# Optimization experiments

Hardware: AMD Instinct MI355X
Metric: run time of the kernel (lower is better)

Reference implementation:

```python
import jax, jax.numpy as jnp
import numpy as np

K = 20  # kNN fan-out


def knn_idx(x, k):
    # x: (B, C, N). Negative squared pairwise distance; top-k largest = nearest.
    inner = -2.0 * jnp.einsum('bcn,bcm->bnm', x, x)        # (B, N, N)
    xx = jnp.sum(x * x, axis=1)                            # (B, N)
    pd = -xx[:, :, None] - inner - xx[:, None, :]          # (B, N, N)
    return jax.lax.top_k(pd, k)[1]                         # (B, N, k) int32


def get_graph_feature(x, k):
    # x: (B, C, N) -> edge features (B, 2C, N, k)
    idx = knn_idx(x, k)                                    # (B, N, k)
    xt = jnp.transpose(x, (0, 2, 1))                       # (B, N, C)
    nbrs = jax.vmap(lambda pts, ids: pts[ids])(xt, idx)    # (B, N, k, C)
    center = xt[:, :, None, :]                             # (B, N, 1, C)
    feat = jnp.concatenate(
        [nbrs - center, jnp.broadcast_to(center, nbrs.shape)], axis=-1)  # (B,N,k,2C)
    return jnp.transpose(feat, (0, 3, 1, 2))               # (B, 2C, N, k)


def vn_layer(W, x):
    # W: (out, in); x: (B, in, N, k) -> (B, out, N, k)
    return jnp.einsum('oi,bink->bonk', W, x)


def setup_inputs() -> dict:
    key = jax.random.key(0)
    ks = jax.random.split(key, 6)
    B, C, N = 16, 3, 2048
    num_classes = 10
    return {
        'x': jax.random.normal(ks[0], (B, C, N), dtype=jnp.float32),
        'W1': jax.random.normal(ks[1], (64, 6), dtype=jnp.float32),
        'W2': jax.random.normal(ks[2], (128, 64), dtype=jnp.float32),
        'W3': jax.random.normal(ks[3], (256, 128), dtype=jnp.float32),
        'fc_w': jax.random.normal(ks[4], (num_classes, 256), dtype=jnp.float32) * 0.0625,
        'fc_b': jax.random.normal(ks[5], (num_classes,), dtype=jnp.float32) * 0.0625,
    }


def reference(x, W1, W2, W3, fc_w, fc_b):
    h = get_graph_feature(x, K)          # (B, 6, N, k)
    h = vn_layer(W1, h)                  # (B, 64, N, k)
    h = jax.nn.relu(vn_layer(W2, h))     # (B, 128, N, k)
    h = jax.nn.relu(vn_layer(W3, h))     # (B, 256, N, k)
    h = jnp.max(h, axis=-1)              # max over neighbors k -> (B, 256, N)
    h = jnp.max(h, axis=-1)              # global max over points -> (B, 256)
    return h @ fc_w.T + fc_b             # (B, num_classes)
```

## Files before the change

kernel.cpp:

```cpp
#include <hip/hip_runtime.h>
#include <stdint.h>

typedef _Float16 v8h __attribute__((ext_vector_type(8)));
typedef _Float16 v2h __attribute__((ext_vector_type(2)));
typedef float v4f __attribute__((ext_vector_type(4)));
typedef float v16f __attribute__((ext_vector_type(16)));

#define NPTS 2048
#define BATCH 16
#define KNN 20
#define PAIRS (NPTS * KNN)

__device__ __forceinline__ unsigned pair_relu_h2(unsigned pu, unsigned qu) {
  v2h a = *(const v2h*)&pu;
  v2h b = *(const v2h*)&qu;
  v2h s = a + b;
  v2h z = {(_Float16)0.f, (_Float16)0.f};
  v2h r = __builtin_elementwise_max(s, z);
  return *(const unsigned*)&r;
}

__global__ void prep_kernel(const float* __restrict__ W1, const float* __restrict__ W2,
                            float* __restrict__ M2a, float* __restrict__ M2b,
                            int* __restrict__ H) {
  if (blockIdx.x == 0 && threadIdx.x < 128) {
    int o = threadIdx.x;
    float a0 = 0, a1 = 0, a2 = 0, b0 = 0, b1 = 0, b2 = 0;
    for (int i = 0; i < 64; ++i) {
      float w2 = W2[o * 64 + i];
      const float* w1r = W1 + i * 6;
      a0 += w2 * w1r[0]; a1 += w2 * w1r[1]; a2 += w2 * w1r[2];
      b0 += w2 * (w1r[3] - w1r[0]); b1 += w2 * (w1r[4] - w1r[1]); b2 += w2 * (w1r[5] - w1r[2]);
    }
    M2a[o * 3 + 0] = a0; M2a[o * 3 + 1] = a1; M2a[o * 3 + 2] = a2;
    M2b[o * 3 + 0] = b0; M2b[o * 3 + 1] = b1; M2b[o * 3 + 2] = b2;
  }
  int g = blockIdx.x * 128 + threadIdx.x;
  if (g < BATCH * 256) H[g] = 0;
}

__global__ __launch_bounds__(64) void pq_kernel(const float* __restrict__ x,
                                                const float* __restrict__ M2a,
                                                const float* __restrict__ M2b,
                                                unsigned short* __restrict__ p,
                                                unsigned short* __restrict__ q) {
  int b = blockIdx.x >> 6;
  int j0 = (blockIdx.x & 63) << 5;
  int t = threadIdx.x;
  int o0 = t * 2;
  float a00 = M2a[o0 * 3 + 0], a01 = M2a[o0 * 3 + 1], a02 = M2a[o0 * 3 + 2];
  float a10 = M2a[o0 * 3 + 3], a11 = M2a[o0 * 3 + 4], a12 = M2a[o0 * 3 + 5];
  float b00 = M2b[o0 * 3 + 0], b01 = M2b[o0 * 3 + 1], b02 = M2b[o0 * 3 + 2];
  float b10 = M2b[o0 * 3 + 3], b11 = M2b[o0 * 3 + 4], b12 = M2b[o0 * 3 + 5];
  const float* xb = x + b * 3 * NPTS;
  unsigned* pw = (unsigned*)p;
  unsigned* qw = (unsigned*)q;
  for (int jj = 0; jj < 32; ++jj) {
    int j = j0 + jj;
    float x0 = xb[j], x1 = xb[NPTS + j], x2 = xb[2 * NPTS + j];
    float p0 = a00 * x0 + a01 * x1 + a02 * x2;
    float p1 = a10 * x0 + a11 * x1 + a12 * x2;
    float q0 = b00 * x0 + b01 * x1 + b02 * x2;
    float q1 = b10 * x0 + b11 * x1 + b12 * x2;
    size_t base = ((size_t)(b * NPTS + j)) * 64 + t;
    auto hp = __builtin_amdgcn_cvt_pkrtz(p0, p1);
    auto hq = __builtin_amdgcn_cvt_pkrtz(q0, q1);
    pw[base] = *(const unsigned*)&hp;
    qw[base] = *(const unsigned*)&hq;
  }
}

__global__ __launch_bounds__(256) void knn_kernel(const float* __restrict__ x,
                                                  int* __restrict__ idxOut) {
  __shared__ float px[NPTS], py[NPTS], pz[NPTS];
  __shared__ unsigned long long cand[4][4][128];
  int b = blockIdx.x >> 7;
  int qblk = blockIdx.x & 127;
  const float* xb = x + b * 3 * NPTS;
  for (int i = threadIdx.x; i < NPTS; i += 256) {
    px[i] = xb[i]; py[i] = xb[NPTS + i]; pz[i] = xb[2 * NPTS + i];
  }
  __syncthreads();
  int wid = threadIdx.x >> 6, lane = threadIdx.x & 63;
  int qbase = qblk * 16 + wid * 4;

  float qx[4], qy[4], qz[4], mn[4];
#pragma unroll
  for (int g = 0; g < 4; ++g) {
    qx[g] = px[qbase + g]; qy[g] = py[qbase + g]; qz[g] = pz[qbase + g];
    mn[g] = 1e30f;
  }

  for (int s = 0; s < 32; ++s) {
    int i = s * 64 + lane;
    float X = px[i], Y = py[i], Z = pz[i];
#pragma unroll
    for (int g = 0; g < 4; ++g) {
      float dx = X - qx[g], dy = Y - qy[g], dz = Z - qz[g];
      mn[g] = fminf(mn[g], dx * dx + dy * dy + dz * dz);
    }
  }

  float tau[4];
#pragma unroll
  for (int g = 0; g < 4; ++g) {
    float v = mn[g];
    for (int k = 2; k <= 64; k <<= 1) {
      for (int j = k >> 1; j > 0; j >>= 1) {
        float o = __shfl_xor(v, j);
        bool low = (lane & j) == 0;
        bool up = (lane & k) == 0;
        v = (low == up) ? fminf(v, o) : fmaxf(v, o);
      }
    }
    tau[g] = __shfl(v, 19) * (1.0f + 3.8e-6f);
  }

  int cnt[4] = {0, 0, 0, 0};
  for (int s = 0; s < 32; ++s) {
    int i = s * 64 + lane;
    float X = px[i], Y = py[i], Z = pz[i];
#pragma unroll
    for (int g = 0; g < 4; ++g) {
      float dx = X - qx[g], dy = Y - qy[g], dz = Z - qz[g];
      float d = dx * dx + dy * dy + dz * dz;
      bool take = d <= tau[g];
      unsigned long long mb = __ballot(take);
      if (take) {
        int pos = cnt[g] + __popcll(mb & ((1ull << lane) - 1ull));
        if (pos < 128)
          cand[wid][g][pos] =
              (((unsigned long long)__float_as_uint(d)) << 32) | (unsigned)i;
      }
      cnt[g] += __popcll(mb);
    }
  }

#pragma unroll
  for (int g = 0; g < 4; ++g) {
    int nc = cnt[g] < 128 ? cnt[g] : 128;
    unsigned long long k0 = (lane < nc) ? cand[wid][g][lane] : ~0ull;
    unsigned long long k1 = (lane + 64 < nc) ? cand[wid][g][lane + 64] : ~0ull;
    int r0 = 0, r1 = 0;
    for (int i = 0; i < nc; ++i) {
      unsigned long long ki = cand[wid][g][i];
      r0 += (ki < k0) ? 1 : 0;
      r1 += (ki < k1) ? 1 : 0;
    }
    long long obase = ((long long)b * NPTS + qbase + g) * KNN;
    if (lane < nc && r0 < KNN) idxOut[obase + r0] = (int)(k0 & 0xffffffffu);
    if (lane + 64 < nc && r1 < KNN) idxOut[obase + r1] = (int)(k1 & 0xffffffffu);
  }
}

__global__ __launch_bounds__(512, 4) void gemm_max_kernel(
    const unsigned short* __restrict__ p, const unsigned short* __restrict__ q,
    const int* __restrict__ idx, const float* __restrict__ W3, int* __restrict__ H) {
  __shared__ __align__(16) unsigned short h2s[2][32 * 128];

  int b = blockIdx.x >> 5;
  int w = blockIdx.x & 31;
  int t = threadIdx.x;
  int lane = t & 63, wid = t >> 6;
  int col = lane & 31, hi = lane >> 5;

  v8h bfr[8];
#pragma unroll
  for (int kk = 0; kk < 8; ++kk) {
    const float* src = W3 + (size_t)(wid * 32 + col) * 128 + kk * 16 + hi * 8;
    v8h f;
#pragma unroll
    for (int jj = 0; jj < 8; ++jj) f[jj] = (_Float16)src[jj];
    bfr[kk] = f;
  }

  const unsigned short* pB = p + (size_t)b * NPTS * 128;
  const unsigned short* qB = q + (size_t)b * NPTS * 128;
  const int* idxB = idx + (size_t)b * PAIRS;

  int pm = t >> 4;
  int cseg = t & 15;
  int stoff = pm * 128 + ((cseg ^ (pm & 7)) * 8);

  uint4 P4n, Q4n;
  {
    int pr = w * 32 + pm;
    int n0 = pr / 20;
    int j0 = idxB[pr] & (NPTS - 1);
    P4n = *(const uint4*)(pB + (size_t)j0 * 128 + cseg * 8);
    Q4n = *(const uint4*)(qB + (size_t)n0 * 128 + cseg * 8);
  }

  float vmx = 0.f;
  int buf = 0;
  for (int T = w; T < PAIRS / 32; T += 32) {
    uint4 R;
    R.x = pair_relu_h2(P4n.x, Q4n.x);
    R.y = pair_relu_h2(P4n.y, Q4n.y);
    R.z = pair_relu_h2(P4n.z, Q4n.z);
    R.w = pair_relu_h2(P4n.w, Q4n.w);
    *(uint4*)&h2s[buf][stoff] = R;
    __syncthreads();

    int Tn = T + 32;
    if (Tn < PAIRS / 32) {
      int prn = Tn * 32 + pm;
      int nn = prn / 20;
      int jn = idxB[prn] & (NPTS - 1);
      P4n = *(const uint4*)(pB + (size_t)jn * 128 + cseg * 8);
      Q4n = *(const uint4*)(qB + (size_t)nn * 128 + cseg * 8);
    }

    v16f acc = {0.f};
#pragma unroll
    for (int kk = 0; kk < 8; ++kk) {
      v8h a = *(const v8h*)&h2s[buf][col * 128 + (((kk * 2 + hi) ^ (col & 7)) * 8)];
      acc = __builtin_amdgcn_mfma_f32_32x32x16_f16(a, bfr[kk], acc, 0, 0, 0);
    }
    float m0 = fmaxf(fmaxf(acc[0], acc[1]), fmaxf(acc[2], acc[3]));
    float m1 = fmaxf(fmaxf(acc[4], acc[5]), fmaxf(acc[6], acc[7]));
    float m2 = fmaxf(fmaxf(acc[8], acc[9]), fmaxf(acc[10], acc[11]));
    float m3 = fmaxf(fmaxf(acc[12], acc[13]), fmaxf(acc[14], acc[15]));
    vmx = fmaxf(vmx, fmaxf(fmaxf(m0, m1), fmaxf(m2, m3)));
    buf ^= 1;
  }

  float vv = fmaxf(vmx, __shfl_xor(vmx, 32));
  if (hi == 0) {
    int ch = wid * 32 + col;
    atomicMax(&H[b * 256 + ch], __float_as_int(vv));
  }
}

__global__ __launch_bounds__(64) void fc_kernel(const int* __restrict__ Hi,
                                                const float* __restrict__ fcw,
                                                const float* __restrict__ fcb,
                                                float* __restrict__ out) {
  int b = blockIdx.x / 10, r = blockIdx.x % 10;
  int lane = threadIdx.x;
  const float* Hb = (const float*)Hi + b * 256;
  float s = 0.f;
#pragma unroll
  for (int c = lane; c < 256; c += 64) s += Hb[c] * fcw[r * 256 + c];
#pragma unroll
  for (int m = 32; m > 0; m >>= 1) s += __shfl_xor(s, m);
  if (lane == 0) out[b * 10 + r] = s + fcb[r];
}

extern "C" void kernel_launch(void* const* d_in, const int* in_sizes, int n_in,
                              void* d_out, int out_size, void* d_ws, size_t ws_size,
                              hipStream_t stream) {
  const float* x   = (const float*)d_in[0];
  const float* W1  = (const float*)d_in[1];
  const float* W2  = (const float*)d_in[2];
  const float* W3  = (const float*)d_in[3];
  const float* fcw = (const float*)d_in[4];
  const float* fcb = (const float*)d_in[5];
  float* out = (float*)d_out;
  char* ws = (char*)d_ws;

  float* M2a = (float*)(ws + 0);
  float* M2b = (float*)(ws + 1536);
  int* H     = (int*)(ws + 4096);
  int* idx   = (int*)(ws + 24576);
  unsigned short* p = (unsigned short*)(ws + 3145728);
  unsigned short* q = (unsigned short*)(ws + 12582912);

  prep_kernel<<<32, 128, 0, stream>>>(W1, W2, M2a, M2b, H);
  pq_kernel<<<BATCH * 64, 64, 0, stream>>>(x, M2a, M2b, p, q);
  knn_kernel<<<BATCH * 128, 256, 0, stream>>>(x, idx);
  gemm_max_kernel<<<BATCH * 32, 512, 0, stream>>>(p, q, idx, W3, H);
  fc_kernel<<<BATCH * 10, 64, 0, stream>>>(H, fcw, fcb, out);
}
```

Measured before the change: 177.4 us.

## Restructure gemm_max to 4 waves with 64 channels each, 48 blocks per batch

The final GEMM+max kernel now uses 256-thread blocks where each wave owns 64 output channels (two MFMA accumulators sharing one A fragment), so each gathered pair tile feeds twice as many MFMAs per LDS read. Grid changes to 48 blocks per batch with batch-interleaved block ordering, and the neighbour index for the next-next tile is prefetched a step earlier to shorten the dependent gather latency. Each thread now gathers two uint4 segments per row. This trades more registers per thread (two B fragment sets, two accumulators) and fewer waves for better operand reuse and better grid fill across CUs.

After: 174.0 us. Within noise of the previous version (-1.9%).

```diff
diff --git a/kernel.cpp b/kernel.cpp
--- a/kernel.cpp
+++ b/kernel.cpp
@@ -153,82 +153,103 @@
   }
 }
 
-__global__ __launch_bounds__(512, 4) void gemm_max_kernel(
+__global__ __launch_bounds__(256, 3) void gemm_max_kernel(
     const unsigned short* __restrict__ p, const unsigned short* __restrict__ q,
     const int* __restrict__ idx, const float* __restrict__ W3, int* __restrict__ H) {
   __shared__ __align__(16) unsigned short h2s[2][32 * 128];
 
-  int b = blockIdx.x >> 5;
-  int w = blockIdx.x & 31;
+  int b = blockIdx.x & 15;
+  int w = blockIdx.x >> 4;
   int t = threadIdx.x;
   int lane = t & 63, wid = t >> 6;
   int col = lane & 31, hi = lane >> 5;
 
-  v8h bfr[8];
+  v8h bfr0[8], bfr1[8];
 #pragma unroll
   for (int kk = 0; kk < 8; ++kk) {
-    const float* src = W3 + (size_t)(wid * 32 + col) * 128 + kk * 16 + hi * 8;
-    v8h f;
-#pragma unroll
-    for (int jj = 0; jj < 8; ++jj) f[jj] = (_Float16)src[jj];
-    bfr[kk] = f;
+    const float* s0 = W3 + (size_t)(wid * 64 + col) * 128 + kk * 16 + hi * 8;
+    const float* s1 = s0 + 32 * 128;
+    v8h f0, f1;
+#pragma unroll
+    for (int jj = 0; jj < 8; ++jj) { f0[jj] = (_Float16)s0[jj]; f1[jj] = (_Float16)s1[jj]; }
+    bfr0[kk] = f0; bfr1[kk] = f1;
   }
 
   const unsigned short* pB = p + (size_t)b * NPTS * 128;
   const unsigned short* qB = q + (size_t)b * NPTS * 128;
   const int* idxB = idx + (size_t)b * PAIRS;
 
-  int pm = t >> 4;
-  int cseg = t & 15;
-  int stoff = pm * 128 + ((cseg ^ (pm & 7)) * 8);
-
-  uint4 P4n, Q4n;
+  int pm = t >> 3;
+  int c2 = t & 7;
+  int st0 = pm * 128 + (((c2 * 2) ^ (pm & 7)) * 8);
+  int st1 = pm * 128 + (((c2 * 2 + 1) ^ (pm & 7)) * 8);
+
+  const int NT = PAIRS / 32;
+
+  uint4 P0, P1, Q0, Q1;
+  int jn = 0;
   {
     int pr = w * 32 + pm;
-    int n0 = pr / 20;
-    int j0 = idxB[pr] & (NPTS - 1);
-    P4n = *(const uint4*)(pB + (size_t)j0 * 128 + cseg * 8);
-    Q4n = *(const uint4*)(qB + (size_t)n0 * 128 + cseg * 8);
-  }
-
-  float vmx = 0.f;
+    int j = idxB[pr] & (NPTS - 1);
+    int n = pr / 20;
+    P0 = *(const uint4*)(pB + (size_t)j * 128 + c2 * 16);
+    P1 = *(const uint4*)(pB + (size_t)j * 128 + c2 * 16 + 8);
+    Q0 = *(const uint4*)(qB + (size_t)n * 128 + c2 * 16);
+    Q1 = *(const uint4*)(qB + (size_t)n * 128 + c2 * 16 + 8);
+    int T1 = w + 48;
+    if (T1 < NT) jn = idxB[T1 * 32 + pm];
+  }
+
+  float vmx0 = 0.f, vmx1 = 0.f;
   int buf = 0;
-  for (int T = w; T < PAIRS / 32; T += 32) {
-    uint4 R;
-    R.x = pair_relu_h2(P4n.x, Q4n.x);
-    R.y = pair_relu_h2(P4n.y, Q4n.y);
-    R.z = pair_relu_h2(P4n.z, Q4n.z);
-    R.w = pair_relu_h2(P4n.w, Q4n.w);
-    *(uint4*)&h2s[buf][stoff] = R;
+  for (int T = w; T < NT; T += 48) {
+    uint4 R0, R1;
+    R0.x = pair_relu_h2(P0.x, Q0.x); R0.y = pair_relu_h2(P0.y, Q0.y);
+    R0.z = pair_relu_h2(P0.z, Q0.z); R0.w = pair_relu_h2(P0.w, Q0.w);
+    R1.x = pair_relu_h2(P1.x, Q1.x); R1.y = pair_relu_h2(P1.y, Q1.y);
+    R1.z = pair_relu_h2(P1.z, Q1.z); R1.w = pair_relu_h2(P1.w, Q1.w);
+    *(uint4*)&h2s[buf][st0] = R0;
+    *(uint4*)&h2s[buf][st1] = R1;
     __syncthreads();
 
-    int Tn = T + 32;
-    if (Tn < PAIRS / 32) {
+    int Tn = T + 48;
+    if (Tn < NT) {
       int prn = Tn * 32 + pm;
-      int nn = prn / 20;
-      int jn = idxB[prn] & (NPTS - 1);
-      P4n = *(const uint4*)(pB + (size_t)jn * 128 + cseg * 8);
-      Q4n = *(const uint4*)(qB + (size_t)nn * 128 + cseg * 8);
-    }
-
-    v16f acc = {0.f};
+      int j = jn & (NPTS - 1);
+      int n = prn / 20;
+      P0 = *(const uint4*)(pB + (size_t)j * 128 + c2 * 16);
+      P1 = *(const uint4*)(pB + (size_t)j * 128 + c2 * 16 + 8);
+      Q0 = *(const uint4*)(qB + (size_t)n * 128 + c2 * 16);
+      Q1 = *(const uint4*)(qB + (size_t)n * 128 + c2 * 16 + 8);
+      int T2 = T + 96;
+      if (T2 < NT) jn = idxB[T2 * 32 + pm];
+    }
+
+    v16f acc0 = {0.f}, acc1 = {0.f};
 #pragma unroll
     for (int kk = 0; kk < 8; ++kk) {
       v8h a = *(const v8h*)&h2s[buf][col * 128 + (((kk * 2 + hi) ^ (col & 7)) * 8)];
-      acc = __builtin_amdgcn_mfma_f32_32x32x16_f16(a, bfr[kk], acc, 0, 0, 0);
-    }
-    float m0 = fmaxf(fmaxf(acc[0], acc[1]), fmaxf(acc[2], acc[3]));
-    float m1 = fmaxf(fmaxf(acc[4], acc[5]), fmaxf(acc[6], acc[7]));
-    float m2 = fmaxf(fmaxf(acc[8], acc[9]), fmaxf(acc[10], acc[11]));
-    float m3 = fmaxf(fmaxf(acc[12], acc[13]), fmaxf(acc[14], acc[15]));
-    vmx = fmaxf(vmx, fmaxf(fmaxf(m0, m1), fmaxf(m2, m3)));
+      acc0 = __builtin_amdgcn_mfma_f32_32x32x16_f16(a, bfr0[kk], acc0, 0, 0, 0);
+      acc1 = __builtin_amdgcn_mfma_f32_32x32x16_f16(a, bfr1[kk], acc1, 0, 0, 0);
+    }
+    float a0 = fmaxf(fmaxf(acc0[0], acc0[1]), fmaxf(acc0[2], acc0[3]));
+    float a1 = fmaxf(fmaxf(acc0[4], acc0[5]), fmaxf(acc0[6], acc0[7]));
+    float a2 = fmaxf(fmaxf(acc0[8], acc0[9]), fmaxf(acc0[10], acc0[11]));
+    float a3 = fmaxf(fmaxf(acc0[12], acc0[13]), fmaxf(acc0[14], acc0[15]));
+    vmx0 = fmaxf(vmx0, fmaxf(fmaxf(a0, a1), fmaxf(a2, a3)));
+    float c0 = fmaxf(fmaxf(acc1[0], acc1[1]), fmaxf(acc1[2], acc1[3]));
+    float c1 = fmaxf(fmaxf(acc1[4], acc1[5]), fmaxf(acc1[6], acc1[7]));
+    float c2v = fmaxf(fmaxf(acc1[8], acc1[9]), fmaxf(acc1[10], acc1[11]));
+    float c3 = fmaxf(fmaxf(acc1[12], acc1[13]), fmaxf(acc1[14], acc1[15]));
+    vmx1 = fmaxf(vmx1, fmaxf(fmaxf(c0, c1), fmaxf(c2v, c3)));
     buf ^= 1;
   }
 
-  float vv = fmaxf(vmx, __shfl_xor(vmx, 32));
+  float v0 = fmaxf(vmx0, __shfl_xor(vmx0, 32));
+  float v1 = fmaxf(vmx1, __shfl_xor(vmx1, 32));
   if (hi == 0) {
-    int ch = wid * 32 + col;
-    atomicMax(&H[b * 256 + ch], __float_as_int(vv));
+    atomicMax(&H[b * 256 + wid * 64 + col], __float_as_int(v0));
+    atomicMax(&H[b * 256 + wid * 64 + 32 + col], __float_as_int(v1));
   }
 }
 
@@ -269,6 +290,6 @@
   prep_kernel<<<32, 128, 0, stream>>>(W1, W2, M2a, M2b, H);
   pq_kernel<<<BATCH * 64, 64, 0, stream>>>(x, M2a, M2b, p, q);
   knn_kernel<<<BATCH * 128, 256, 0, stream>>>(x, idx);
-  gemm_max_kernel<<<BATCH * 32, 512, 0, stream>>>(p, q, idx, W3, H);
+  gemm_max_kernel<<<BATCH * 48, 256, 0, stream>>>(p, q, idx, W3, H);
   fc_kernel<<<BATCH * 10, 64, 0, stream>>>(H, fcw, fcb, out);
 }
```
